# Performance work log

Hardware: AMD Instinct MI355X
Metric: run time of the kernel (lower is better)

Reference implementation:

```python
import jax, jax.numpy as jnp
import numpy as np

EMBED_DIM = 1024
NUM_HEADS = 16
HEAD_DIM = EMBED_DIM // NUM_HEADS
ROPE_BASE = 10000.0


def _rope_angles(seq_len, head_dim):
    inv_freq = 1.0 / (ROPE_BASE ** (jnp.arange(0, head_dim, 2, dtype=jnp.float32) / head_dim))  # [D/2]
    pos = jnp.arange(seq_len, dtype=jnp.float32)
    ang = pos[:, None] * inv_freq[None, :]  # [S, D/2]
    return jnp.cos(ang), jnp.sin(ang)


def _apply_rope(t, cos, sin):
    # t: [B, H, S, D]; rotate-half convention
    d2 = t.shape[-1] // 2
    t1, t2 = t[..., :d2], t[..., d2:]
    return jnp.concatenate([t1 * cos - t2 * sin, t2 * cos + t1 * sin], axis=-1)


def setup_inputs() -> dict:
    key = jax.random.key(0)
    ks = jax.random.split(key, 6)
    B, S, E = 1, 4096, EMBED_DIM
    x = jax.random.normal(ks[0], (B, S, E), dtype=jnp.float32)
    # causal mask: True means masked-out (upper triangle above diagonal)
    mask = jnp.triu(jnp.ones((S, S), dtype=bool), k=1)[None, None, :, :]
    scale = 0.02
    wqkv_w = jax.random.normal(ks[1], (E, 3 * E), dtype=jnp.float32) * scale
    wqkv_b = jax.random.normal(ks[2], (3 * E,), dtype=jnp.float32) * scale
    out_w = jax.random.normal(ks[3], (E, E), dtype=jnp.float32) * scale
    out_b = jax.random.normal(ks[4], (E,), dtype=jnp.float32) * scale
    return {"x": x, "mask": mask, "wqkv_w": wqkv_w, "wqkv_b": wqkv_b, "out_w": out_w, "out_b": out_b}


def reference(x, mask, wqkv_w, wqkv_b, out_w, out_b):
    B, S, E = x.shape
    H, D = NUM_HEADS, HEAD_DIM
    qkv = x @ wqkv_w + wqkv_b  # [B, S, 3E]
    q, k, v = jnp.split(qkv, 3, axis=-1)
    # [B, S, E] -> [B, H, S, D]
    q = q.reshape(B, S, H, D).transpose(0, 2, 1, 3)
    k = k.reshape(B, S, H, D).transpose(0, 2, 1, 3)
    v = v.reshape(B, S, H, D).transpose(0, 2, 1, 3)
    cos, sin = _rope_angles(S, D)  # [S, D/2]
    q = _apply_rope(q, cos, sin)
    k = _apply_rope(k, cos, sin)
    scores = jnp.einsum('bhqd,bhkd->bhqk', q, k) * (D ** -0.5)  # [B, H, S, S]
    scores = jnp.where(mask[:, :, -S:, :], -jnp.inf, scores)
    weights = jax.nn.softmax(scores, axis=-1)
    ctx = jnp.einsum('bhqk,bhkd->bhqd', weights, v)  # [B, H, S, D]
    ctx = ctx.transpose(0, 2, 1, 3).reshape(B, S, E)
    return ctx @ out_w + out_b
```

## Files before the change

kernel.cpp:

```cpp
#include <hip/hip_runtime.h>
#include <hip/hip_bf16.h>
#include <math.h>

#define S_LEN 4096
#define EMB   1024
#define E3    3072
#define NH    16
#define HD    64

typedef unsigned short u16;
typedef short          bfrag __attribute__((ext_vector_type(8)));
typedef float          ffrag __attribute__((ext_vector_type(4)));
typedef unsigned short us8   __attribute__((ext_vector_type(8)));
typedef unsigned short us4   __attribute__((ext_vector_type(4)));

__device__ __forceinline__ u16 f2bf(float f) {
    union { float f; unsigned u; } v; v.f = f;
    unsigned r = v.u + 0x7fffu + ((v.u >> 16) & 1u);
    return (u16)(r >> 16);
}
__device__ __forceinline__ unsigned pack_bf16_trunc(float lo, float hi) {
    union { float f; unsigned u; } a, b; a.f = lo; b.f = hi;
    return __builtin_amdgcn_perm(b.u, a.u, 0x07060302u);
}
__device__ __forceinline__ void gld16(const void* g, void* l) {
    __builtin_amdgcn_global_load_lds(
        (const __attribute__((address_space(1))) unsigned int*)g,
        (__attribute__((address_space(3))) unsigned int*)l, 16, 0, 0);
}

__global__ __launch_bounds__(256)
void cast_bf16_kernel(const float* __restrict__ in, u16* __restrict__ out) {
    const size_t i = ((size_t)blockIdx.x * 256 + threadIdx.x) * 8;
    float4 a = *(const float4*)(in + i);
    float4 b = *(const float4*)(in + i + 4);
    us8 o;
    o[0]=f2bf(a.x); o[1]=f2bf(a.y); o[2]=f2bf(a.z); o[3]=f2bf(a.w);
    o[4]=f2bf(b.x); o[5]=f2bf(b.y); o[6]=f2bf(b.z); o[7]=f2bf(b.w);
    *(us8*)(out + i) = o;
}

__global__ __launch_bounds__(256)
void transpose_cast_kernel(const float* __restrict__ in, u16* __restrict__ out,
                           int R, int C) {
    __shared__ u16 T[64][72];
    const int r0 = blockIdx.x * 64, c0 = blockIdx.y * 64;
    const int t = threadIdx.x;
    const int rr = t >> 2, cc = (t & 3) * 16;

    const float* ip = in + (size_t)(r0 + rr) * C + c0 + cc;
    u16 tmp[16];
    #pragma unroll
    for (int i4 = 0; i4 < 4; i4++) {
        float4 v = ((const float4*)ip)[i4];
        tmp[4*i4+0]=f2bf(v.x); tmp[4*i4+1]=f2bf(v.y);
        tmp[4*i4+2]=f2bf(v.z); tmp[4*i4+3]=f2bf(v.w);
    }
    #pragma unroll
    for (int i8 = 0; i8 < 2; i8++) {
        us8 vv;
        #pragma unroll
        for (int j = 0; j < 8; j++) vv[j] = tmp[8*i8+j];
        *(us8*)&T[rr][cc + 8*i8] = vv;
    }
    __syncthreads();

    const int oc = t >> 2, orr = (t & 3) * 16;
    u16 ot[16];
    #pragma unroll
    for (int j = 0; j < 16; j++) ot[j] = T[orr + j][oc];
    u16* op = out + (size_t)(c0 + oc) * R + r0 + orr;
    #pragma unroll
    for (int i8 = 0; i8 < 2; i8++) {
        us8 vv;
        #pragma unroll
        for (int j = 0; j < 8; j++) vv[j] = ot[8*i8+j];
        *(us8*)(op + 8*i8) = vv;
    }
}

__global__ __launch_bounds__(256)
void transpose_v_kernel(const u16* __restrict__ qkvb, u16* __restrict__ vt) {
    __shared__ u16 T[64][72];
    const int s0 = blockIdx.x * 64, h = blockIdx.y;
    const int t = threadIdx.x;
    const int rr = t >> 2, cc = (t & 3) * 16;

    const u16* ip = qkvb + (size_t)(s0 + rr) * E3 + 2 * EMB + h * HD + cc;
    *(us8*)&T[rr][cc]     = *(const us8*)ip;
    *(us8*)&T[rr][cc + 8] = *(const us8*)(ip + 8);
    __syncthreads();

    const int od = t >> 2, os = (t & 3) * 16;
    u16 ot[16];
    #pragma unroll
    for (int j = 0; j < 16; j++) ot[j] = T[os + j][od];
    u16* op = vt + ((size_t)h * HD + od) * S_LEN + s0 + os;
    #pragma unroll
    for (int i8 = 0; i8 < 2; i8++) {
        us8 vv;
        #pragma unroll
        for (int j = 0; j < 8; j++) vv[j] = ot[8*i8+j];
        *(us8*)(op + 8*i8) = vv;
    }
}

template <int OUT_BF16, int NT, int ROPE, int MINW>
__global__ __launch_bounds__(256, MINW)
void gemm_bt_kernel(const u16* __restrict__ A, const u16* __restrict__ Bt,
                    const float* __restrict__ bias, void* __restrict__ Cv,
                    int M, int N, int K) {
    constexpr int BN = 32 * NT;
    constexpr int WS = 16 * NT;
    __shared__ u16 As[2][128][32];
    __shared__ u16 Bs[2][BN][32];

    const int tid = threadIdx.x;
    const int w = tid >> 6, L = tid & 63;
    const int col = L & 15, quad = L >> 4;
    const int wm = w & 1, wn = w >> 1;
    const int m0 = blockIdx.x * 128, n0 = blockIdx.y * BN;

    ffrag acc[4][NT];
    #pragma unroll
    for (int a = 0; a < 4; a++)
        #pragma unroll
        for (int b = 0; b < NT; b++)
            #pragma unroll
            for (int r = 0; r < 4; r++) acc[a][b][r] = 0.f;

    const int srow = L >> 2;
    const int schk = L & 3;

    #pragma unroll
    for (int t = 0; t < 2; t++) {
        const int rg = (2 * w + t) * 16;
        gld16(A + (size_t)(m0 + rg + srow) * K + schk * 8, &As[0][rg][0]);
    }
    #pragma unroll
    for (int t = 0; t < NT / 2; t++) {
        const int rg = (w * (NT / 2) + t) * 16;
        gld16(Bt + (size_t)(n0 + rg + srow) * K + schk * 8, &Bs[0][rg][0]);
    }
    __syncthreads();

    int buf = 0;
    for (int k0 = 0; k0 < K; k0 += 32, buf ^= 1) {
        if (k0 + 32 < K) {
            #pragma unroll
            for (int t = 0; t < 2; t++) {
                const int rg = (2 * w + t) * 16;
                gld16(A + (size_t)(m0 + rg + srow) * K + k0 + 32 + schk * 8,
                      &As[buf ^ 1][rg][0]);
            }
            #pragma unroll
            for (int t = 0; t < NT / 2; t++) {
                const int rg = (w * (NT / 2) + t) * 16;
                gld16(Bt + (size_t)(n0 + rg + srow) * K + k0 + 32 + schk * 8,
                      &Bs[buf ^ 1][rg][0]);
            }
        }

        bfrag af[4], bf[NT];
        #pragma unroll
        for (int mt = 0; mt < 4; mt++)
            af[mt] = *(const bfrag*)&As[buf][64 * wm + 16 * mt + col][8 * quad];
        #pragma unroll
        for (int nt = 0; nt < NT; nt++)
            bf[nt] = *(const bfrag*)&Bs[buf][WS * wn + 16 * nt + col][8 * quad];
        #pragma unroll
        for (int mt = 0; mt < 4; mt++)
            #pragma unroll
            for (int nt = 0; nt < NT; nt++)
                acc[mt][nt] = __builtin_amdgcn_mfma_f32_16x16x32_bf16(
                    af[mt], bf[nt], acc[mt][nt], 0, 0, 0);

        __syncthreads();
    }

    float bv[NT];
    #pragma unroll
    for (int nt = 0; nt < NT; nt++) bv[nt] = bias[n0 + WS * wn + 16 * nt + col];

    if (ROPE && n0 < 2 * EMB) {
        const float SCq = (n0 < EMB) ? 0.125f * 1.44269504088896f : 1.0f;
        const float C = 13.287712379549449f / 32.0f;
        float invf[2];
        invf[0] = exp2f(-(float)col * C);
        invf[1] = exp2f(-(float)(col + 16) * C);
        #pragma unroll
        for (int mt = 0; mt < 4; mt++) {
            #pragma unroll
            for (int r = 0; r < 4; r++) {
                const int mrow = m0 + 64 * wm + 16 * mt + 4 * quad + r;
                const float fs = (float)mrow;
                u16* cp = (u16*)Cv + (size_t)mrow * N + n0 + 64 * wn + col;
                #pragma unroll
                for (int pr = 0; pr < 2; pr++) {
                    float sn, cs;
                    sincosf(fs * invf[pr], &sn, &cs);
                    const float t1 = acc[mt][pr][r] + bv[pr];
                    const float t2 = acc[mt][pr + 2][r] + bv[pr + 2];
                    cp[16 * pr]      = f2bf((t1 * cs - t2 * sn) * SCq);
                    cp[16 * pr + 32] = f2bf((t2 * cs + t1 * sn) * SCq);
                }
            }
        }
    } else {
        #pragma unroll
        for (int mt = 0; mt < 4; mt++) {
            #pragma unroll
            for (int r = 0; r < 4; r++) {
                const int m = m0 + 64 * wm + 16 * mt + 4 * quad + r;
                #pragma unroll
                for (int nt = 0; nt < NT; nt++) {
                    const int n = n0 + WS * wn + 16 * nt + col;
                    const float val = acc[mt][nt][r] + bv[nt];
                    if (OUT_BF16) ((u16*)Cv)[(size_t)m * N + n] = f2bf(val);
                    else          ((float*)Cv)[(size_t)m * N + n] = val;
                }
            }
        }
    }
}

__global__ __launch_bounds__(256, 2)
void flash6_kernel(const u16* __restrict__ qkvb, const u16* __restrict__ vt,
                   u16* __restrict__ ctxb) {
    __shared__ u16 QP[4][32][64];
    __shared__ u16 Ks[2][64][64];
    __shared__ u16 Vs[2][64][64];

    const int id = blockIdx.x;
    const int j  = (id >> 3) & 31;
    const int hi = id >> 8;
    const int h  = (id & 7) | (hi << 3);
    const int zig = (j < 16) ? j : 47 - j;
    const int qi  = hi ? (31 - zig) : zig;
    const int q0  = qi * 128;
    const int ntk = 2 * qi + 2;

    const int tid = threadIdx.x;
    const int w = tid >> 6, L = tid & 63;
    const int col = L & 15, quad = L >> 4;
    const int lr = L >> 3, lp = L & 7;
    const int lc = lp ^ lr;

    const int nwt = ntk - (w < 2 ? 1 : 0);

    const size_t kArow = (size_t)(16 * w + lr) * E3 + EMB + h * HD + lc * 8;
    const size_t vArow = ((size_t)h * HD + 16 * w + lr) * S_LEN + lc * 8;

    #pragma unroll
    for (int u = 0; u < 4; u++)
        gld16(qkvb + (size_t)(q0 + 32 * w + 8 * u + lr) * E3 + h * HD + lc * 8,
              &QP[w][8 * u][0]);
    #pragma unroll
    for (int u = 0; u < 2; u++) {
        gld16(qkvb + kArow + (size_t)(8 * u) * E3, &Ks[0][16 * w + 8 * u][0]);
        gld16(vt + vArow + (size_t)(8 * u) * S_LEN, &Vs[0][16 * w + 8 * u][0]);
    }
    __syncthreads();

    bfrag qf[2][2];
    #pragma unroll
    for (int i = 0; i < 2; i++)
        #pragma unroll
        for (int ks = 0; ks < 2; ks++)
            qf[i][ks] = *(const bfrag*)
                ((const char*)&QP[w][16 * i + col][0] +
                 16 * ((4 * ks + quad) ^ (col & 7)));

    bfrag ones;
    #pragma unroll
    for (int i = 0; i < 8; i++) ones[i] = (short)0x3F80;

    ffrag o[4][2], ol[2];
    #pragma unroll
    for (int d4 = 0; d4 < 4; d4++)
        #pragma unroll
        for (int i = 0; i < 2; i++)
            #pragma unroll
            for (int r = 0; r < 4; r++) o[d4][i][r] = 0.f;
    #pragma unroll
    for (int i = 0; i < 2; i++)
        #pragma unroll
        for (int r = 0; r < 4; r++) ol[i][r] = 0.f;

    #pragma unroll 1
    for (int t = 0; t < ntk; t++) {
        const int buf = t & 1;
        if (t + 1 < ntk) {
            const size_t ko = kArow + (size_t)(t + 1) * 64 * E3;
            const size_t vo = vArow + (size_t)(t + 1) * 64;
            #pragma unroll
            for (int u = 0; u < 2; u++) {
                gld16(qkvb + ko + (size_t)(8 * u) * E3,
                      &Ks[buf ^ 1][16 * w + 8 * u][0]);
                gld16(vt + vo + (size_t)(8 * u) * S_LEN,
                      &Vs[buf ^ 1][16 * w + 8 * u][0]);
            }
        }

        if (t < nwt) {
            ffrag st[4][2];
            #pragma unroll
            for (int t4 = 0; t4 < 4; t4++)
                #pragma unroll
                for (int i = 0; i < 2; i++)
                    #pragma unroll
                    for (int r = 0; r < 4; r++) st[t4][i][r] = 0.f;
            #pragma unroll
            for (int ks = 0; ks < 2; ks++) {
                bfrag kf[4];
                #pragma unroll
                for (int t4 = 0; t4 < 4; t4++)
                    kf[t4] = *(const bfrag*)
                        &Ks[buf][16 * t4 + col][(((4 * ks + quad) ^ (col & 7)) * 8)];
                #pragma unroll
                for (int t4 = 0; t4 < 4; t4++)
                    #pragma unroll
                    for (int i = 0; i < 2; i++)
                        st[t4][i] = __builtin_amdgcn_mfma_f32_16x16x32_bf16(
                            kf[t4], qf[i][ks], st[t4][i], 0, 0, 0);
            }

            if (t == nwt - 1) {
                #pragma unroll
                for (int i = 0; i < 2; i++) {
                    const int qrel = 32 * (w & 1) + 16 * i + col;
                    #pragma unroll
                    for (int t4 = 0; t4 < 4; t4++) {
                        const int key0 = 16 * t4 + 4 * quad;
                        #pragma unroll
                        for (int r = 0; r < 4; r++)
                            if (key0 + r > qrel) st[t4][i][r] = -3.0e38f;
                    }
                }
            }

            #pragma unroll
            for (int i = 0; i < 2; i++) {
                const int prow = 16 * i + col;
                #pragma unroll
                for (int t4 = 0; t4 < 4; t4++) {
                    float pr[4];
                    #pragma unroll
                    for (int r = 0; r < 4; r++) pr[r] = exp2f(st[t4][i][r]);
                    uint2 pk;
                    pk.x = pack_bf16_trunc(pr[0], pr[1]);
                    pk.y = pack_bf16_trunc(pr[2], pr[3]);
                    const int c2 = (2 * t4 + (quad >> 1)) ^ (col & 7);
                    *(uint2*)((char*)&QP[w][prow][0] + 16 * c2 + 8 * (quad & 1)) = pk;
                }
            }

            #pragma unroll
            for (int ks = 0; ks < 2; ks++) {
                bfrag vf[4];
                #pragma unroll
                for (int d4 = 0; d4 < 4; d4++)
                    vf[d4] = *(const bfrag*)
                        &Vs[buf][16 * d4 + col][(((4 * ks + quad) ^ (col & 7)) * 8)];
                bfrag pf[2];
                #pragma unroll
                for (int i = 0; i < 2; i++)
                    pf[i] = *(const bfrag*)
                        ((const char*)&QP[w][16 * i + col][0] +
                         16 * ((4 * ks + quad) ^ (col & 7)));
                #pragma unroll
                for (int d4 = 0; d4 < 4; d4++)
                    #pragma unroll
                    for (int i = 0; i < 2; i++)
                        o[d4][i] = __builtin_amdgcn_mfma_f32_16x16x32_bf16(
                            vf[d4], pf[i], o[d4][i], 0, 0, 0);
                #pragma unroll
                for (int i = 0; i < 2; i++)
                    ol[i] = __builtin_amdgcn_mfma_f32_16x16x32_bf16(
                        ones, pf[i], ol[i], 0, 0, 0);
            }
        }

        __syncthreads();
    }

    #pragma unroll
    for (int i = 0; i < 2; i++) {
        const float inv = 1.0f / ol[i][0];
        const int qg = q0 + 32 * w + 16 * i + col;
        #pragma unroll
        for (int d4 = 0; d4 < 4; d4++) {
            us4 pk;
            #pragma unroll
            for (int r = 0; r < 4; r++) pk[r] = f2bf(o[d4][i][r] * inv);
            *(us4*)&ctxb[(size_t)qg * EMB + h * HD + 16 * d4 + 4 * quad] = pk;
        }
    }
}

extern "C" void kernel_launch(void* const* d_in, const int* in_sizes, int n_in,
                              void* d_out, int out_size, void* d_ws, size_t ws_size,
                              hipStream_t stream) {
    const float* x      = (const float*)d_in[0];
    const float* wqkv_w = (const float*)d_in[2];
    const float* wqkv_b = (const float*)d_in[3];
    const float* out_w  = (const float*)d_in[4];
    const float* out_b  = (const float*)d_in[5];
    float* out = (float*)d_out;

    u16* qkvb = (u16*)d_ws;
    u16* ctxb = qkvb + (size_t)S_LEN * E3;
    u16* xb   = ctxb + (size_t)S_LEN * EMB;
    u16* wt   = xb   + (size_t)S_LEN * EMB;
    u16* owt  = wt   + (size_t)E3 * EMB;
    u16* vtb  = owt  + (size_t)EMB * EMB;

    dim3 blk(256);

    cast_bf16_kernel<<<dim3(S_LEN * EMB / (256 * 8)), blk, 0, stream>>>(x, xb);
    transpose_cast_kernel<<<dim3(EMB / 64, E3 / 64), blk, 0, stream>>>(
        wqkv_w, wt, EMB, E3);
    transpose_cast_kernel<<<dim3(EMB / 64, EMB / 64), blk, 0, stream>>>(
        out_w, owt, EMB, EMB);

    gemm_bt_kernel<1, 4, 1, 3><<<dim3(S_LEN / 128, E3 / 128), blk, 0, stream>>>(
        xb, wt, wqkv_b, qkvb, S_LEN, E3, EMB);

    transpose_v_kernel<<<dim3(S_LEN / 64, NH), blk, 0, stream>>>(qkvb, vtb);

    flash6_kernel<<<dim3(512), blk, 0, stream>>>(qkvb, vtb, ctxb);

    gemm_bt_kernel<0, 2, 0, 2><<<dim3(S_LEN / 128, EMB / 64), blk, 0, stream>>>(
        ctxb, owt, out_b, out, S_LEN, EMB, EMB);
}
```

Baseline: 257.5 us.

## Fuse V transpose into QKV GEMM epilogue and shrink flash blocks to 64 queries

The QKV GEMM epilogue now writes the V third of its output directly in transposed [h*d, s] layout, which removes the separate transpose_v kernel and its extra pass over V. The flash attention kernel is restructured to 128-thread blocks covering 64 queries each, launched as 1024 blocks with a new interleaved ordering of query tiles per head. This drops the per-wave tile skipping and gives finer causal load balance and more blocks in flight, at the cost of more K/V reloads per query and strided 8-byte stores in the GEMM epilogue.

```diff
diff --git a/kernel.cpp b/kernel.cpp
--- a/kernel.cpp
+++ b/kernel.cpp
@@ -79,37 +79,11 @@
     }
 }
 
-__global__ __launch_bounds__(256)
-void transpose_v_kernel(const u16* __restrict__ qkvb, u16* __restrict__ vt) {
-    __shared__ u16 T[64][72];
-    const int s0 = blockIdx.x * 64, h = blockIdx.y;
-    const int t = threadIdx.x;
-    const int rr = t >> 2, cc = (t & 3) * 16;
-
-    const u16* ip = qkvb + (size_t)(s0 + rr) * E3 + 2 * EMB + h * HD + cc;
-    *(us8*)&T[rr][cc]     = *(const us8*)ip;
-    *(us8*)&T[rr][cc + 8] = *(const us8*)(ip + 8);
-    __syncthreads();
-
-    const int od = t >> 2, os = (t & 3) * 16;
-    u16 ot[16];
-    #pragma unroll
-    for (int j = 0; j < 16; j++) ot[j] = T[os + j][od];
-    u16* op = vt + ((size_t)h * HD + od) * S_LEN + s0 + os;
-    #pragma unroll
-    for (int i8 = 0; i8 < 2; i8++) {
-        us8 vv;
-        #pragma unroll
-        for (int j = 0; j < 8; j++) vv[j] = ot[8*i8+j];
-        *(us8*)(op + 8*i8) = vv;
-    }
-}
-
 template <int OUT_BF16, int NT, int ROPE, int MINW>
 __global__ __launch_bounds__(256, MINW)
 void gemm_bt_kernel(const u16* __restrict__ A, const u16* __restrict__ Bt,
                     const float* __restrict__ bias, void* __restrict__ Cv,
-                    int M, int N, int K) {
+                    u16* __restrict__ vtp, int M, int N, int K) {
     constexpr int BN = 32 * NT;
     constexpr int WS = 16 * NT;
     __shared__ u16 As[2][128][32];
@@ -206,6 +180,19 @@
                 }
             }
         }
+    } else if (ROPE) {
+        #pragma unroll
+        for (int nt = 0; nt < NT; nt++) {
+            const int dg = n0 - 2 * EMB + WS * wn + 16 * nt + col;
+            #pragma unroll
+            for (int mt = 0; mt < 4; mt++) {
+                const int s0 = m0 + 64 * wm + 16 * mt + 4 * quad;
+                us4 pk;
+                #pragma unroll
+                for (int r = 0; r < 4; r++) pk[r] = f2bf(acc[mt][nt][r] + bv[nt]);
+                *(us4*)&vtp[(size_t)dg * S_LEN + s0] = pk;
+            }
+        }
     } else {
         #pragma unroll
         for (int mt = 0; mt < 4; mt++) {
@@ -224,21 +211,24 @@
     }
 }
 
-__global__ __launch_bounds__(256, 2)
-void flash6_kernel(const u16* __restrict__ qkvb, const u16* __restrict__ vt,
+__global__ __launch_bounds__(128, 2)
+void flash7_kernel(const u16* __restrict__ qkvb, const u16* __restrict__ vt,
                    u16* __restrict__ ctxb) {
-    __shared__ u16 QP[4][32][64];
+    __shared__ u16 QP[2][32][64];
     __shared__ u16 Ks[2][64][64];
     __shared__ u16 Vs[2][64][64];
 
     const int id = blockIdx.x;
-    const int j  = (id >> 3) & 31;
-    const int hi = id >> 8;
-    const int h  = (id & 7) | (hi << 3);
-    const int zig = (j < 16) ? j : 47 - j;
-    const int qi  = hi ? (31 - zig) : zig;
-    const int q0  = qi * 128;
-    const int ntk = 2 * qi + 2;
+    const int h  = (id & 7) | (((id >> 3) & 1) << 3);
+    const int a  = (id >> 4) & 15;
+    const int b  = id >> 8;
+    int qi;
+    if      (b == 0) qi = 2 * a;
+    else if (b == 1) qi = 63 - 2 * a;
+    else if (b == 2) qi = 2 * a + 1;
+    else             qi = 62 - 2 * a;
+    const int q0 = qi * 64;
+    const int ntk = qi + 1;
 
     const int tid = threadIdx.x;
     const int w = tid >> 6, L = tid & 63;
@@ -246,19 +236,15 @@
     const int lr = L >> 3, lp = L & 7;
     const int lc = lp ^ lr;
 
-    const int nwt = ntk - (w < 2 ? 1 : 0);
-
-    const size_t kArow = (size_t)(16 * w + lr) * E3 + EMB + h * HD + lc * 8;
-    const size_t vArow = ((size_t)h * HD + 16 * w + lr) * S_LEN + lc * 8;
-
-    #pragma unroll
-    for (int u = 0; u < 4; u++)
+    const size_t kArow = (size_t)(32 * w + lr) * E3 + EMB + h * HD + lc * 8;
+    const size_t vArow = ((size_t)h * HD + 32 * w + lr) * S_LEN + lc * 8;
+
+    #pragma unroll
+    for (int u = 0; u < 4; u++) {
         gld16(qkvb + (size_t)(q0 + 32 * w + 8 * u + lr) * E3 + h * HD + lc * 8,
               &QP[w][8 * u][0]);
-    #pragma unroll
-    for (int u = 0; u < 2; u++) {
-        gld16(qkvb + kArow + (size_t)(8 * u) * E3, &Ks[0][16 * w + 8 * u][0]);
-        gld16(vt + vArow + (size_t)(8 * u) * S_LEN, &Vs[0][16 * w + 8 * u][0]);
+        gld16(qkvb + kArow + (size_t)(8 * u) * E3, &Ks[0][32 * w + 8 * u][0]);
+        gld16(vt + vArow + (size_t)(8 * u) * S_LEN, &Vs[0][32 * w + 8 * u][0]);
     }
     __syncthreads();
 
@@ -294,91 +280,89 @@
             const size_t ko = kArow + (size_t)(t + 1) * 64 * E3;
             const size_t vo = vArow + (size_t)(t + 1) * 64;
             #pragma unroll
-            for (int u = 0; u < 2; u++) {
+            for (int u = 0; u < 4; u++) {
                 gld16(qkvb + ko + (size_t)(8 * u) * E3,
-                      &Ks[buf ^ 1][16 * w + 8 * u][0]);
+                      &Ks[buf ^ 1][32 * w + 8 * u][0]);
                 gld16(vt + vo + (size_t)(8 * u) * S_LEN,
-                      &Vs[buf ^ 1][16 * w + 8 * u][0]);
-            }
-        }
-
-        if (t < nwt) {
-            ffrag st[4][2];
+                      &Vs[buf ^ 1][32 * w + 8 * u][0]);
+            }
+        }
+
+        ffrag st[4][2];
+        #pragma unroll
+        for (int t4 = 0; t4 < 4; t4++)
+            #pragma unroll
+            for (int i = 0; i < 2; i++)
+                #pragma unroll
+                for (int r = 0; r < 4; r++) st[t4][i][r] = 0.f;
+        #pragma unroll
+        for (int ks = 0; ks < 2; ks++) {
+            bfrag kf[4];
             #pragma unroll
             for (int t4 = 0; t4 < 4; t4++)
+                kf[t4] = *(const bfrag*)
+                    &Ks[buf][16 * t4 + col][(((4 * ks + quad) ^ (col & 7)) * 8)];
+            #pragma unroll
+            for (int t4 = 0; t4 < 4; t4++)
                 #pragma unroll
                 for (int i = 0; i < 2; i++)
+                    st[t4][i] = __builtin_amdgcn_mfma_f32_16x16x32_bf16(
+                        kf[t4], qf[i][ks], st[t4][i], 0, 0, 0);
+        }
+
+        if (t == ntk - 1) {
+            #pragma unroll
+            for (int i = 0; i < 2; i++) {
+                const int qrel = 32 * w + 16 * i + col;
+                #pragma unroll
+                for (int t4 = 0; t4 < 4; t4++) {
+                    const int key0 = 16 * t4 + 4 * quad;
                     #pragma unroll
-                    for (int r = 0; r < 4; r++) st[t4][i][r] = 0.f;
-            #pragma unroll
-            for (int ks = 0; ks < 2; ks++) {
-                bfrag kf[4];
-                #pragma unroll
-                for (int t4 = 0; t4 < 4; t4++)
-                    kf[t4] = *(const bfrag*)
-                        &Ks[buf][16 * t4 + col][(((4 * ks + quad) ^ (col & 7)) * 8)];
-                #pragma unroll
-                for (int t4 = 0; t4 < 4; t4++)
-                    #pragma unroll
-                    for (int i = 0; i < 2; i++)
-                        st[t4][i] = __builtin_amdgcn_mfma_f32_16x16x32_bf16(
-                            kf[t4], qf[i][ks], st[t4][i], 0, 0, 0);
-            }
-
-            if (t == nwt - 1) {
-                #pragma unroll
-                for (int i = 0; i < 2; i++) {
-                    const int qrel = 32 * (w & 1) + 16 * i + col;
-                    #pragma unroll
-                    for (int t4 = 0; t4 < 4; t4++) {
-                        const int key0 = 16 * t4 + 4 * quad;
-                        #pragma unroll
-                        for (int r = 0; r < 4; r++)
-                            if (key0 + r > qrel) st[t4][i][r] = -3.0e38f;
-                    }
+                    for (int r = 0; r < 4; r++)
+                        if (key0 + r > qrel) st[t4][i][r] = -3.0e38f;
                 }
             }
-
-            #pragma unroll
-            for (int i = 0; i < 2; i++) {
-                const int prow = 16 * i + col;
-                #pragma unroll
-                for (int t4 = 0; t4 < 4; t4++) {
-                    float pr[4];
-                    #pragma unroll
-                    for (int r = 0; r < 4; r++) pr[r] = exp2f(st[t4][i][r]);
-                    uint2 pk;
-                    pk.x = pack_bf16_trunc(pr[0], pr[1]);
-                    pk.y = pack_bf16_trunc(pr[2], pr[3]);
-                    const int c2 = (2 * t4 + (quad >> 1)) ^ (col & 7);
-                    *(uint2*)((char*)&QP[w][prow][0] + 16 * c2 + 8 * (quad & 1)) = pk;
-                }
-            }
-
-            #pragma unroll
-            for (int ks = 0; ks < 2; ks++) {
-                bfrag vf[4];
-                #pragma unroll
-                for (int d4 = 0; d4 < 4; d4++)
-                    vf[d4] = *(const bfrag*)
-                        &Vs[buf][16 * d4 + col][(((4 * ks + quad) ^ (col & 7)) * 8)];
-                bfrag pf[2];
+        }
+
+        #pragma unroll
+        for (int i = 0; i < 2; i++) {
+            const int prow = 16 * i + col;
+            #pragma unroll
+            for (int t4 = 0; t4 < 4; t4++) {
+                float pr[4];
+                #pragma unroll
+                for (int r = 0; r < 4; r++) pr[r] = exp2f(st[t4][i][r]);
+                uint2 pk;
+                pk.x = pack_bf16_trunc(pr[0], pr[1]);
+                pk.y = pack_bf16_trunc(pr[2], pr[3]);
+                const int c2 = (2 * t4 + (quad >> 1)) ^ (col & 7);
+                *(uint2*)((char*)&QP[w][prow][0] + 16 * c2 + 8 * (quad & 1)) = pk;
+            }
+        }
+
+        #pragma unroll
+        for (int ks = 0; ks < 2; ks++) {
+            bfrag vf[4];
+            #pragma unroll
+            for (int d4 = 0; d4 < 4; d4++)
+                vf[d4] = *(const bfrag*)
+                    &Vs[buf][16 * d4 + col][(((4 * ks + quad) ^ (col & 7)) * 8)];
+            bfrag pf[2];
+            #pragma unroll
+            for (int i = 0; i < 2; i++)
+                pf[i] = *(const bfrag*)
+                    ((const char*)&QP[w][16 * i + col][0] +
+                     16 * ((4 * ks + quad) ^ (col & 7)));
+            #pragma unroll
+            for (int d4 = 0; d4 < 4; d4++)
                 #pragma unroll
                 for (int i = 0; i < 2; i++)
-                    pf[i] = *(const bfrag*)
-                        ((const char*)&QP[w][16 * i + col][0] +
-                         16 * ((4 * ks + quad) ^ (col & 7)));
-                #pragma unroll
-                for (int d4 = 0; d4 < 4; d4++)
-                    #pragma unroll
-                    for (int i = 0; i < 2; i++)
-                        o[d4][i] = __builtin_amdgcn_mfma_f32_16x16x32_bf16(
-                            vf[d4], pf[i], o[d4][i], 0, 0, 0);
-                #pragma unroll
-                for (int i = 0; i < 2; i++)
-                    ol[i] = __builtin_amdgcn_mfma_f32_16x16x32_bf16(
-                        ones, pf[i], ol[i], 0, 0, 0);
-            }
+                    o[d4][i] = __builtin_amdgcn_mfma_f32_16x16x32_bf16(
+                        vf[d4], pf[i], o[d4][i], 0, 0, 0);
+            #pragma unroll
+            for (int i = 0; i < 2; i++)
+                ol[i] = __builtin_amdgcn_mfma_f32_16x16x32_bf16(
+                    ones, pf[i], ol[i], 0, 0, 0);
         }
 
         __syncthreads();
@@ -424,12 +408,10 @@
         out_w, owt, EMB, EMB);
 
     gemm_bt_kernel<1, 4, 1, 3><<<dim3(S_LEN / 128, E3 / 128), blk, 0, stream>>>(
-        xb, wt, wqkv_b, qkvb, S_LEN, E3, EMB);
-
-    transpose_v_kernel<<<dim3(S_LEN / 64, NH), blk, 0, stream>>>(qkvb, vtb);
-
-    flash6_kernel<<<dim3(512), blk, 0, stream>>>(qkvb, vtb, ctxb);
+        xb, wt, wqkv_b, qkvb, vtb, S_LEN, E3, EMB);
+
+    flash7_kernel<<<dim3(1024), dim3(128), 0, stream>>>(qkvb, vtb, ctxb);
 
     gemm_bt_kernel<0, 2, 0, 2><<<dim3(S_LEN / 128, EMB / 64), blk, 0, stream>>>(
-        ctxb, owt, out_b, out, S_LEN, EMB, EMB);
-}
+        ctxb, owt, out_b, out, nullptr, S_LEN, EMB, EMB);
+}
```

After: 269.8 us. 1.05x slower.
